# Optimization experiments

Measured on AMD Instinct MI355X. Metric: run time of the kernel, lower is better.

The kernel has to match this reference:

```python
import jax, jax.numpy as jnp
import numpy as np

N_NODES = 100000
N_EDGES = 1600000
HIDDEN = 128
N_GRAPHS = 64
N_CLASSES = 10


def setup_inputs() -> dict:
    key = jax.random.key(0)
    ks = jax.random.split(key, 10)
    x = jax.random.normal(ks[0], (N_NODES, 1), dtype=jnp.float32)
    edge_index = jax.random.randint(ks[1], (2, N_EDGES), 0, N_NODES, dtype=jnp.int32)
    batch = jnp.sort(jax.random.randint(ks[2], (N_NODES,), 0, N_GRAPHS, dtype=jnp.int32))
    def glorot(k, shape):
        fan_in, fan_out = shape
        s = jnp.sqrt(6.0 / (fan_in + fan_out))
        return jax.random.uniform(k, shape, jnp.float32, -s, s)
    return {
        "x": x,
        "edge_index": edge_index,
        "batch": batch,
        "W1l": glorot(ks[3], (1, HIDDEN)),
        "W1r": glorot(ks[4], (1, HIDDEN)),
        "b1": jnp.zeros((HIDDEN,), jnp.float32),
        "W2l": glorot(ks[5], (HIDDEN, HIDDEN)),
        "W2r": glorot(ks[6], (HIDDEN, HIDDEN)),
        "b2": jnp.zeros((HIDDEN,), jnp.float32),
        "W3l": glorot(ks[7], (HIDDEN, HIDDEN)),
        "W3r": glorot(ks[8], (HIDDEN, HIDDEN)),
        "b3": jnp.zeros((HIDDEN,), jnp.float32),
        "Wfc": glorot(ks[9], (HIDDEN, N_CLASSES)),
        "bfc": jnp.zeros((N_CLASSES,), jnp.float32),
    }


def _sage_conv(x, src, dst, Wl, Wr, b, n_nodes):
    # mean aggregation of source features at destination nodes
    msg = x[src]                                              # [E, d_in]
    agg = jax.ops.segment_sum(msg, dst, num_segments=n_nodes)  # [N, d_in]
    cnt = jax.ops.segment_sum(jnp.ones((src.shape[0], 1), x.dtype), dst,
                              num_segments=n_nodes)            # [N, 1]
    mean = agg / jnp.maximum(cnt, 1.0)
    # PyG SAGEConv: lin_l(mean neighbors) + bias + lin_r(self)
    return mean @ Wl + b + x @ Wr


def reference(x, edge_index, batch, W1l, W1r, b1, W2l, W2r, b2,
              W3l, W3r, b3, Wfc, bfc):
    src, dst = edge_index[0], edge_index[1]
    n = x.shape[0]
    h = jax.nn.relu(_sage_conv(x, src, dst, W1l, W1r, b1, n))
    h = jax.nn.relu(_sage_conv(h, src, dst, W2l, W2r, b2, n))
    h = jax.nn.relu(_sage_conv(h, src, dst, W3l, W3r, b3, n))
    # global_mean_pool over graph ids in `batch`
    pooled = jax.ops.segment_sum(h, batch, num_segments=N_GRAPHS)
    gcnt = jax.ops.segment_sum(jnp.ones((n, 1), h.dtype), batch,
                               num_segments=N_GRAPHS)
    pooled = pooled / jnp.maximum(gcnt, 1.0)
    logits = pooled @ Wfc + bfc
    return jax.nn.log_softmax(logits, axis=1)
```

## Files before the change

### kernel.cpp

```cpp
#include <hip/hip_runtime.h>

typedef unsigned int u32;
typedef unsigned short u16;
typedef short bf16x8 __attribute__((ext_vector_type(8)));
typedef float f32x4 __attribute__((ext_vector_type(4)));
typedef float f32x2 __attribute__((ext_vector_type(2)));
typedef u32 u32x4 __attribute__((ext_vector_type(4)));

#define HBLK 256

__device__ __forceinline__ u16 f2bf(float f) {
  u32 u = __float_as_uint(f);
  u = (u + 0x7FFFu + ((u >> 16) & 1u)) >> 16;
  return (u16)u;
}
__device__ __forceinline__ float bf2f(u32 h) { return __uint_as_float(h << 16); }

__global__ void hist_wprep_kernel(const int* __restrict__ dst, int* __restrict__ boff,
                                  int* __restrict__ btotal, int E, int nbuk, int chunk,
                                  const float* __restrict__ W2l, const float* __restrict__ W2r,
                                  const float* __restrict__ W3l, const float* __restrict__ W3r,
                                  u16* __restrict__ wt2, u16* __restrict__ wt3,
                                  const int* __restrict__ batch, int* __restrict__ gcnt, int n) {
  int tid = threadIdx.x;
  int idx = blockIdx.x * 1024 + tid;
  if (idx < 65536) {
    int which = idx >> 15, r = idx & 32767;
    int j = r >> 8, k = r & 255;
    if (which == 0) {
      float v = (k < 128) ? W2l[k * 128 + j] : W2r[(k - 128) * 128 + j];
      wt2[r] = f2bf(v);
    } else {
      float v = (k < 128) ? W3l[k * 128 + j] : W3r[(k - 128) * 128 + j];
      wt3[r] = f2bf(v);
    }
  }
  __shared__ int h[1024];
  __shared__ int gh[64];
  for (int i = tid; i < nbuk; i += 1024) h[i] = 0;
  if (tid < 64) gh[tid] = 0;
  __syncthreads();
  int b0 = blockIdx.x * chunk, b1 = min(b0 + chunk, E);
  int len = max(b1 - b0, 0);
  int ng = len >> 2;
  for (int g4 = tid; g4 < ng; g4 += 1024) {
    u32x4 d4 = *(const u32x4*)(dst + b0 + g4 * 4);
#pragma unroll
    for (int w = 0; w < 4; ++w) atomicAdd(&h[(int)d4[w] >> 7], 1);
  }
  for (int e = b0 + ng * 4 + tid; e < b1; e += 1024)
    atomicAdd(&h[dst[e] >> 7], 1);
  int chunkN = (n + HBLK - 1) / HBLK;
  int n0 = blockIdx.x * chunkN, n1 = min(n0 + chunkN, n);
  for (int i = n0 + tid; i < n1; i += 1024)
    atomicAdd(&gh[batch[i]], 1);
  __syncthreads();
  for (int i = tid; i < nbuk; i += 1024)
    boff[i * HBLK + blockIdx.x] = atomicAdd(&btotal[i], h[i]);
  if (tid < 64 && gh[tid] > 0)
    atomicAdd(&gcnt[tid], gh[tid]);
}

__global__ void scatter2_kernel(const int* __restrict__ src, const int* __restrict__ dst,
                                const int* __restrict__ btotal, const int* __restrict__ boff,
                                u32* __restrict__ part, int* __restrict__ bbase,
                                int E, int nbuk, int chunk) {
  __shared__ int wsum[1024];
  __shared__ int cur[1024];
  int tid = threadIdx.x;
  int v = (tid < nbuk) ? btotal[tid] : 0;
  wsum[tid] = v;
  __syncthreads();
  for (int off = 1; off < 1024; off <<= 1) {
    int t = (tid >= off) ? wsum[tid - off] : 0;
    __syncthreads();
    wsum[tid] += t;
    __syncthreads();
  }
  int excl = wsum[tid] - v;
  if (tid < nbuk) {
    cur[tid] = excl + boff[tid * HBLK + blockIdx.x];
    if (blockIdx.x == 0) bbase[tid] = excl;
  }
  __syncthreads();
  int b0 = blockIdx.x * chunk, b1 = min(b0 + chunk, E);
  int len = max(b1 - b0, 0);
  int ng = len >> 2;
  for (int g4 = tid; g4 < ng; g4 += 1024) {
    int e = b0 + g4 * 4;
    u32x4 s4 = *(const u32x4*)(src + e);
    u32x4 d4 = *(const u32x4*)(dst + e);
#pragma unroll
    for (int w = 0; w < 4; ++w) {
      int d = (int)d4[w];
      int pos = atomicAdd(&cur[d >> 7], 1);
      part[pos] = s4[w] | ((u32)(d & 127) << 25);
    }
  }
  for (int e = b0 + ng * 4 + tid; e < b1; e += 1024) {
    int d = dst[e];
    int pos = atomicAdd(&cur[d >> 7], 1);
    part[pos] = (u32)src[e] | ((u32)(d & 127) << 25);
  }
}

__global__ void scatter3_kernel(const u32* __restrict__ part, const int* __restrict__ bbase,
                                const float* __restrict__ x,
                                const float* __restrict__ W1l, const float* __restrict__ W1r,
                                const float* __restrict__ b1,
                                int* __restrict__ roff, int* __restrict__ csr,
                                u32* __restrict__ h1, int E, int nbuk, int n) {
  int b = blockIdx.x;
  int tid = threadIdx.x;
  int base = bbase[b];
  int end = (b + 1 < nbuk) ? bbase[b + 1] : E;
  __shared__ int cnt[128];
  __shared__ int s[128];
  __shared__ int cur[128];
  __shared__ float xsum[128];
  __shared__ float meanv[128];
  __shared__ float wlA[128], wrA[128], bA[128];
  if (tid < 128) {
    cnt[tid] = 0; xsum[tid] = 0.f;
    wlA[tid] = W1l[tid]; wrA[tid] = W1r[tid]; bA[tid] = b1[tid];
  }
  __syncthreads();
  for (int e = base + tid; e < end; e += 512)
    atomicAdd(&cnt[part[e] >> 25], 1);
  __syncthreads();
  if (tid < 128) s[tid] = cnt[tid];
  __syncthreads();
  for (int off = 1; off < 128; off <<= 1) {
    int t = (tid >= off && tid < 128) ? s[tid - off] : 0;
    __syncthreads();
    if (tid < 128) s[tid] += t;
    __syncthreads();
  }
  if (tid < 128) {
    int excl = s[tid] - cnt[tid];
    cur[tid] = base + excl;
    int node = b * 128 + tid;
    if (node < n) roff[node] = base + excl;
  }
  if (b == 0 && tid == 0) roff[n] = E;
  __syncthreads();
  for (int e = base + tid; e < end; e += 512) {
    u32 p = part[e];
    int sidx = (int)(p & 0x1FFFFFFu);
    int pos = atomicAdd(&cur[p >> 25], 1);
    csr[pos] = sidx;
    atomicAdd(&xsum[p >> 25], x[sidx]);
  }
  __syncthreads();
  if (tid < 128) meanv[tid] = xsum[tid] / (float)max(cnt[tid], 1);
  __syncthreads();
  int nlocal = min(128, n - b * 128);
  for (int q = tid; q < nlocal * 64; q += 512) {
    int ln = q >> 6, w = q & 63;
    int node = b * 128 + ln;
    int j0 = w * 2;
    float m = meanv[ln], xs = x[node];
    float v0 = fmaxf(m * wlA[j0] + xs * wrA[j0] + bA[j0], 0.f);
    float v1 = fmaxf(m * wlA[j0 + 1] + xs * wrA[j0 + 1] + bA[j0 + 1], 0.f);
    h1[(size_t)node * 64 + w] = (u32)f2bf(v0) | ((u32)f2bf(v1) << 16);
  }
}

__device__ __forceinline__ u32x4 grow(const u32* hp, int s) {
  return *(const u32x4*)(hp + (size_t)s * 64);
}
__device__ __forceinline__ void acc_row(f32x2* a, u32x4 v) {
#pragma unroll
  for (int w = 0; w < 4; ++w)
    a[w] += (f32x2){bf2f(v[w] & 0xFFFFu), bf2f(v[w] >> 16)};
}

__global__ void agg_kernel(const int* __restrict__ csr, const int* __restrict__ roff,
                           const u32* __restrict__ hin, u32* __restrict__ outv, int n) {
  int g = threadIdx.x >> 4, li = threadIdx.x & 15;
  int i = blockIdx.x * 16 + g;
  if (i >= n) return;
  int e0 = roff[i], e1 = roff[i + 1];
  f32x2 a[4] = {};
  const u32* hp = hin + li * 4;
  int e = e0;
  for (; e + 7 < e1; e += 8) {
    int s0 = csr[e], s1 = csr[e + 1], s2 = csr[e + 2], s3 = csr[e + 3];
    int s4 = csr[e + 4], s5 = csr[e + 5], s6 = csr[e + 6], s7 = csr[e + 7];
    u32x4 v0 = grow(hp, s0), v1 = grow(hp, s1), v2 = grow(hp, s2), v3 = grow(hp, s3);
    u32x4 v4 = grow(hp, s4), v5 = grow(hp, s5), v6 = grow(hp, s6), v7 = grow(hp, s7);
    acc_row(a, v0); acc_row(a, v1); acc_row(a, v2); acc_row(a, v3);
    acc_row(a, v4); acc_row(a, v5); acc_row(a, v6); acc_row(a, v7);
  }
  for (; e + 3 < e1; e += 4) {
    int s0 = csr[e], s1 = csr[e + 1], s2 = csr[e + 2], s3 = csr[e + 3];
    u32x4 v0 = grow(hp, s0), v1 = grow(hp, s1), v2 = grow(hp, s2), v3 = grow(hp, s3);
    acc_row(a, v0); acc_row(a, v1); acc_row(a, v2); acc_row(a, v3);
  }
  for (; e < e1; ++e) acc_row(a, grow(hp, csr[e]));
  float inv = 1.f / (float)max(e1 - e0, 1);
  u32x4 o;
#pragma unroll
  for (int w = 0; w < 4; ++w)
    o[w] = (u32)f2bf(a[w].x * inv) | ((u32)f2bf(a[w].y * inv) << 16);
  *(u32x4*)(outv + (size_t)i * 64 + li * 4) = o;
}

template <int MODE>
__launch_bounds__(512)
__global__ void mm_kernel(const u16* Aleft, const u16* Aright,
                          const u16* __restrict__ Wt, const float* __restrict__ bias,
                          u16* Out, const int* __restrict__ batch,
                          float* __restrict__ pooled, int n) {
  __shared__ u16 wlds[32768];
  __shared__ int bgp[128];
  for (int c = threadIdx.x; c < 4096; c += 512) {
    int j = c >> 5, ch = c & 31;
    int swz = ch ^ (j & 31);
    *(u32x4*)(&wlds[j * 256 + swz * 8]) = *(const u32x4*)(&Wt[j * 256 + ch * 8]);
  }
  __syncthreads();
  int wave = threadIdx.x >> 6;
  int lane = threadIdx.x & 63;
  int quad = lane >> 4, l16 = lane & 15;
  int row0 = blockIdx.x * 128 + wave * 16;
  int m = row0 + l16;
  int mc = m < n ? m : (n - 1);
  f32x4 acc[8] = {};
  const u16* Ah[2] = {Aleft, Aright};
#pragma unroll
  for (int half = 0; half < 2; ++half) {
    const u16* A = Ah[half] + (size_t)mc * 128;
#pragma unroll
    for (int s = 0; s < 4; ++s) {
      bf16x8 a = *(const bf16x8*)(A + s * 32 + quad * 8);
      int chunk = (half << 4) + (s << 2) + quad;
#pragma unroll
      for (int t = 0; t < 8; ++t) {
        int j = t * 16 + l16;
        int swz = chunk ^ (j & 31);
        bf16x8 b = *(const bf16x8*)(&wlds[j * 256 + swz * 8]);
        acc[t] = __builtin_amdgcn_mfma_f32_16x16x32_bf16(a, b, acc[t], 0, 0, 0);
      }
    }
  }
  __syncthreads();
  int rl_base = wave * 16 + quad * 4;
#pragma unroll
  for (int t = 0; t < 8; ++t) {
    int j = t * 16 + l16;
    float bj = bias[j];
#pragma unroll
    for (int r = 0; r < 4; ++r) {
      float v = acc[t][r] + bj;
      wlds[(rl_base + r) * 136 + j] = f2bf(fmaxf(v, 0.f));
    }
  }
  if (MODE == 1) {
    if (threadIdx.x < 128) {
      int rr = blockIdx.x * 128 + threadIdx.x;
      bgp[threadIdx.x] = (rr < n) ? batch[rr] : -1;
    }
  }
  __syncthreads();
  if (MODE == 0) {
    int base_row = blockIdx.x * 128;
    for (int q = 0; q < 4; ++q) {
      int idx = q * 512 + threadIdx.x;
      int rl = idx >> 4;
      int ch = idx & 15;
      int mr = base_row + rl;
      if (mr < n)
        *(u32x4*)(&Out[(size_t)mr * 128 + ch * 8]) =
            *(const u32x4*)(&wlds[rl * 136 + ch * 8]);
    }
  } else {
    int tcol = threadIdx.x & 127, seg = threadIdx.x >> 7;
    float accp = 0.f;
    int gcur = -1;
    for (int r = seg * 32; r < seg * 32 + 32; ++r) {
      int gb = bgp[r];
      if (gb != gcur) {
        if (gcur >= 0) atomicAdd(&pooled[gcur * 128 + tcol], accp);
        gcur = gb;
        accp = 0.f;
      }
      if (gb >= 0) accp += bf2f((u32)wlds[r * 136 + tcol]);
    }
    if (gcur >= 0) atomicAdd(&pooled[gcur * 128 + tcol], accp);
  }
}

__global__ void head_kernel(const float* __restrict__ pooled, const int* __restrict__ gcnt,
                            const float* __restrict__ Wfc, const float* __restrict__ bfc,
                            float* __restrict__ out) {
  __shared__ float lg[64][10];
  int t = threadIdx.x;
  if (t < 640) {
    int g = t / 10, c = t % 10;
    float inv = 1.f / (float)max(gcnt[g], 1);
    float acc = bfc[c];
    for (int k = 0; k < 128; ++k) acc += pooled[g * 128 + k] * inv * Wfc[k * 10 + c];
    lg[g][c] = acc;
  }
  __syncthreads();
  if (t < 640) {
    int g = t / 10, c = t % 10;
    float mx = -1e30f;
    for (int q = 0; q < 10; ++q) mx = fmaxf(mx, lg[g][q]);
    float se = 0.f;
    for (int q = 0; q < 10; ++q) se += expf(lg[g][q] - mx);
    out[g * 10 + c] = lg[g][c] - mx - logf(se);
  }
}

extern "C" void kernel_launch(void* const* d_in, const int* in_sizes, int n_in,
                              void* d_out, int out_size, void* d_ws, size_t ws_size,
                              hipStream_t stream) {
  const float* x   = (const float*)d_in[0];
  const int* ei    = (const int*)d_in[1];
  const int* batch = (const int*)d_in[2];
  const float* W1l = (const float*)d_in[3];
  const float* W1r = (const float*)d_in[4];
  const float* b1  = (const float*)d_in[5];
  const float* W2l = (const float*)d_in[6];
  const float* W2r = (const float*)d_in[7];
  const float* b2  = (const float*)d_in[8];
  const float* W3l = (const float*)d_in[9];
  const float* W3r = (const float*)d_in[10];
  const float* b3  = (const float*)d_in[11];
  const float* Wfc = (const float*)d_in[12];
  const float* bfc = (const float*)d_in[13];
  float* out = (float*)d_out;
  int N = in_sizes[0];
  int E = in_sizes[1] / 2;
  const int* src = ei;
  const int* dst = ei + E;

  char* p = (char*)d_ws;
  auto alloc = [&](size_t bytes) { void* r = (void*)p; p += (bytes + 255) & ~(size_t)255; return r; };
  int* roff   = (int*)alloc((size_t)(N + 1) * 4);
  int* csr    = (int*)alloc((size_t)E * 4);
  u32* bufA   = (u32*)alloc((size_t)N * 64 * 4);
  u32* bufB   = (u32*)alloc((size_t)N * 64 * 4);
  u16* wt2    = (u16*)alloc(32768 * 2);
  u16* wt3    = (u16*)alloc(32768 * 2);
  float* pooled = (float*)alloc(64 * 128 * 4);
  int* gcnt   = (int*)alloc(64 * 4);
  int* btotal = (int*)alloc(1024 * 4);
  int* bbase  = (int*)alloc(1024 * 4);

  int nbuk = (N + 127) >> 7;
  int* boff = (int*)bufA;
  u32* part = (u32*)bufB;
  int chunk = (((E + HBLK - 1) / HBLK) + 3) & ~3;

  hipMemsetAsync(pooled, 0, 32768 + 256 + 4096, stream);
  hist_wprep_kernel<<<HBLK, 1024, 0, stream>>>(dst, boff, btotal, E, nbuk, chunk,
                                               W2l, W2r, W3l, W3r, wt2, wt3,
                                               batch, gcnt, N);
  scatter2_kernel<<<HBLK, 1024, 0, stream>>>(src, dst, btotal, boff, part, bbase,
                                             E, nbuk, chunk);
  scatter3_kernel<<<nbuk, 512, 0, stream>>>(part, bbase, x, W1l, W1r, b1,
                                            roff, csr, bufA, E, nbuk, N);
  agg_kernel<<<(N + 15) / 16, 256, 0, stream>>>(csr, roff, bufA, bufB, N);
  mm_kernel<0><<<(N + 127) / 128, 512, 0, stream>>>((const u16*)bufB, (const u16*)bufA,
                                                    wt2, b2, (u16*)bufB, batch, pooled, N);
  agg_kernel<<<(N + 15) / 16, 256, 0, stream>>>(csr, roff, bufB, bufA, N);
  mm_kernel<1><<<(N + 127) / 128, 512, 0, stream>>>((const u16*)bufA, (const u16*)bufB,
                                                    wt3, b3, (u16*)bufA, batch, pooled, N);
  head_kernel<<<1, 640, 0, stream>>>(pooled, gcnt, Wfc, bfc, out);
}
```

Measured before the change: 300.5 us.

## Build CSR via per-node global atomics degree histogram and direct scatter

Replaces the two-level bucketed CSR construction (shared-memory bucket histogram, partitioned packed edges, per-bucket local sort) with a flat per-node degree histogram in global memory. A two-pass block scan over degrees produces row offsets, and a single scatter pass places edges using global atomics on per-node cursors while accumulating the layer-1 x sums. The layer-1 dense transform moves into its own kernel. This drops the intermediate partition buffer and one pass over the edges, but every edge now does global atomics with random addresses, which can serialize or thrash L2.

```diff
diff --git a/kernel.cpp b/kernel.cpp
--- a/kernel.cpp
+++ b/kernel.cpp
@@ -16,8 +16,9 @@
 }
 __device__ __forceinline__ float bf2f(u32 h) { return __uint_as_float(h << 16); }
 
-__global__ void hist_wprep_kernel(const int* __restrict__ dst, int* __restrict__ boff,
-                                  int* __restrict__ btotal, int E, int nbuk, int chunk,
+
+__global__ void hist_wprep_kernel(const int* __restrict__ dst, int* __restrict__ deg,
+                                  int E, int chunk,
                                   const float* __restrict__ W2l, const float* __restrict__ W2r,
                                   const float* __restrict__ W3l, const float* __restrict__ W3r,
                                   u16* __restrict__ wt2, u16* __restrict__ wt3,
@@ -35,9 +36,7 @@
       wt3[r] = f2bf(v);
     }
   }
-  __shared__ int h[1024];
   __shared__ int gh[64];
-  for (int i = tid; i < nbuk; i += 1024) h[i] = 0;
   if (tid < 64) gh[tid] = 0;
   __syncthreads();
   int b0 = blockIdx.x * chunk, b1 = min(b0 + chunk, E);
@@ -46,43 +45,65 @@
   for (int g4 = tid; g4 < ng; g4 += 1024) {
     u32x4 d4 = *(const u32x4*)(dst + b0 + g4 * 4);
 #pragma unroll
-    for (int w = 0; w < 4; ++w) atomicAdd(&h[(int)d4[w] >> 7], 1);
+    for (int w = 0; w < 4; ++w) atomicAdd(&deg[(int)d4[w]], 1);
   }
   for (int e = b0 + ng * 4 + tid; e < b1; e += 1024)
-    atomicAdd(&h[dst[e] >> 7], 1);
+    atomicAdd(&deg[dst[e]], 1);
   int chunkN = (n + HBLK - 1) / HBLK;
   int n0 = blockIdx.x * chunkN, n1 = min(n0 + chunkN, n);
   for (int i = n0 + tid; i < n1; i += 1024)
     atomicAdd(&gh[batch[i]], 1);
   __syncthreads();
-  for (int i = tid; i < nbuk; i += 1024)
-    boff[i * HBLK + blockIdx.x] = atomicAdd(&btotal[i], h[i]);
   if (tid < 64 && gh[tid] > 0)
     atomicAdd(&gcnt[tid], gh[tid]);
 }
 
-__global__ void scatter2_kernel(const int* __restrict__ src, const int* __restrict__ dst,
-                                const int* __restrict__ btotal, const int* __restrict__ boff,
-                                u32* __restrict__ part, int* __restrict__ bbase,
-                                int E, int nbuk, int chunk) {
-  __shared__ int wsum[1024];
-  __shared__ int cur[1024];
-  int tid = threadIdx.x;
-  int v = (tid < nbuk) ? btotal[tid] : 0;
-  wsum[tid] = v;
+__global__ void degsum_kernel(const int* __restrict__ deg, int* __restrict__ bsum, int n) {
+  __shared__ int s[1024];
+  int tid = threadIdx.x;
+  int node = blockIdx.x * 1024 + tid;
+  s[tid] = (node < n) ? deg[node] : 0;
+  __syncthreads();
+  for (int off = 512; off > 0; off >>= 1) {
+    if (tid < off) s[tid] += s[tid + off];
+    __syncthreads();
+  }
+  if (tid == 0) bsum[blockIdx.x] = s[0];
+}
+
+__global__ void degscan_kernel(const int* __restrict__ deg, const int* __restrict__ bsum,
+                               int* __restrict__ roff, int* __restrict__ cur,
+                               int nb, int n, int E) {
+  __shared__ int s[1024];
+  __shared__ int bs[256];
+  int tid = threadIdx.x;
+  if (tid < nb) bs[tid] = bsum[tid];
+  int node = blockIdx.x * 1024 + tid;
+  int v = (node < n) ? deg[node] : 0;
+  s[tid] = v;
   __syncthreads();
   for (int off = 1; off < 1024; off <<= 1) {
-    int t = (tid >= off) ? wsum[tid - off] : 0;
+    int t = (tid >= off) ? s[tid - off] : 0;
     __syncthreads();
-    wsum[tid] += t;
+    s[tid] += t;
     __syncthreads();
   }
-  int excl = wsum[tid] - v;
-  if (tid < nbuk) {
-    cur[tid] = excl + boff[tid * HBLK + blockIdx.x];
-    if (blockIdx.x == 0) bbase[tid] = excl;
-  }
-  __syncthreads();
+  int base = 0;
+  for (int i = 0; i < blockIdx.x; ++i) base += bs[i];
+  int incl = s[tid];
+  int excl = incl - v;
+  if (node < n) {
+    roff[node] = base + excl;
+    cur[node] = base + excl;
+  }
+  if (node == n - 1) roff[n] = base + incl;
+}
+
+__global__ void scatter_kernel(const int* __restrict__ src, const int* __restrict__ dst,
+                               const float* __restrict__ x, int* __restrict__ cur,
+                               int* __restrict__ csr, float* __restrict__ xsum,
+                               int E, int chunk) {
+  int tid = threadIdx.x;
   int b0 = blockIdx.x * chunk, b1 = min(b0 + chunk, E);
   int len = max(b1 - b0, 0);
   int ng = len >> 2;
@@ -92,77 +113,45 @@
     u32x4 d4 = *(const u32x4*)(dst + e);
 #pragma unroll
     for (int w = 0; w < 4; ++w) {
-      int d = (int)d4[w];
-      int pos = atomicAdd(&cur[d >> 7], 1);
-      part[pos] = s4[w] | ((u32)(d & 127) << 25);
+      int d = (int)d4[w], si = (int)s4[w];
+      int pos = atomicAdd(&cur[d], 1);
+      csr[pos] = si;
+      atomicAdd(&xsum[d], x[si]);
     }
   }
   for (int e = b0 + ng * 4 + tid; e < b1; e += 1024) {
-    int d = dst[e];
-    int pos = atomicAdd(&cur[d >> 7], 1);
-    part[pos] = (u32)src[e] | ((u32)(d & 127) << 25);
-  }
-}
-
-__global__ void scatter3_kernel(const u32* __restrict__ part, const int* __restrict__ bbase,
-                                const float* __restrict__ x,
-                                const float* __restrict__ W1l, const float* __restrict__ W1r,
-                                const float* __restrict__ b1,
-                                int* __restrict__ roff, int* __restrict__ csr,
-                                u32* __restrict__ h1, int E, int nbuk, int n) {
-  int b = blockIdx.x;
-  int tid = threadIdx.x;
-  int base = bbase[b];
-  int end = (b + 1 < nbuk) ? bbase[b + 1] : E;
-  __shared__ int cnt[128];
-  __shared__ int s[128];
-  __shared__ int cur[128];
-  __shared__ float xsum[128];
-  __shared__ float meanv[128];
+    int d = dst[e], si = src[e];
+    int pos = atomicAdd(&cur[d], 1);
+    csr[pos] = si;
+    atomicAdd(&xsum[d], x[si]);
+  }
+}
+
+__global__ void l1_kernel(const float* __restrict__ x, const float* __restrict__ xsum,
+                          const int* __restrict__ deg,
+                          const float* __restrict__ W1l, const float* __restrict__ W1r,
+                          const float* __restrict__ b1, u32* __restrict__ h1, int n) {
   __shared__ float wlA[128], wrA[128], bA[128];
+  __shared__ float meanv[128], xv[128];
+  int tid = threadIdx.x;
+  int base = blockIdx.x * 128;
+  int nlocal = min(128, n - base);
   if (tid < 128) {
-    cnt[tid] = 0; xsum[tid] = 0.f;
     wlA[tid] = W1l[tid]; wrA[tid] = W1r[tid]; bA[tid] = b1[tid];
-  }
-  __syncthreads();
-  for (int e = base + tid; e < end; e += 512)
-    atomicAdd(&cnt[part[e] >> 25], 1);
-  __syncthreads();
-  if (tid < 128) s[tid] = cnt[tid];
-  __syncthreads();
-  for (int off = 1; off < 128; off <<= 1) {
-    int t = (tid >= off && tid < 128) ? s[tid - off] : 0;
-    __syncthreads();
-    if (tid < 128) s[tid] += t;
-    __syncthreads();
-  }
-  if (tid < 128) {
-    int excl = s[tid] - cnt[tid];
-    cur[tid] = base + excl;
-    int node = b * 128 + tid;
-    if (node < n) roff[node] = base + excl;
-  }
-  if (b == 0 && tid == 0) roff[n] = E;
-  __syncthreads();
-  for (int e = base + tid; e < end; e += 512) {
-    u32 p = part[e];
-    int sidx = (int)(p & 0x1FFFFFFu);
-    int pos = atomicAdd(&cur[p >> 25], 1);
-    csr[pos] = sidx;
-    atomicAdd(&xsum[p >> 25], x[sidx]);
-  }
-  __syncthreads();
-  if (tid < 128) meanv[tid] = xsum[tid] / (float)max(cnt[tid], 1);
-  __syncthreads();
-  int nlocal = min(128, n - b * 128);
-  for (int q = tid; q < nlocal * 64; q += 512) {
+    if (tid < nlocal) {
+      int node = base + tid;
+      meanv[tid] = xsum[node] / (float)max(deg[node], 1);
+      xv[tid] = x[node];
+    }
+  }
+  __syncthreads();
+  for (int q = tid; q < nlocal * 64; q += 256) {
     int ln = q >> 6, w = q & 63;
-    int node = b * 128 + ln;
     int j0 = w * 2;
-    float m = meanv[ln], xs = x[node];
+    float m = meanv[ln], xs = xv[ln];
     float v0 = fmaxf(m * wlA[j0] + xs * wrA[j0] + bA[j0], 0.f);
     float v1 = fmaxf(m * wlA[j0 + 1] + xs * wrA[j0 + 1] + bA[j0 + 1], 0.f);
-    h1[(size_t)node * 64 + w] = (u32)f2bf(v0) | ((u32)f2bf(v1) << 16);
+    h1[(size_t)(base + ln) * 64 + w] = (u32)f2bf(v0) | ((u32)f2bf(v1) << 16);
   }
 }
 
@@ -346,23 +335,24 @@
   u16* wt2    = (u16*)alloc(32768 * 2);
   u16* wt3    = (u16*)alloc(32768 * 2);
   float* pooled = (float*)alloc(64 * 128 * 4);
-  int* gcnt   = (int*)alloc(64 * 4);
-  int* btotal = (int*)alloc(1024 * 4);
-  int* bbase  = (int*)alloc(1024 * 4);
-
-  int nbuk = (N + 127) >> 7;
-  int* boff = (int*)bufA;
-  u32* part = (u32*)bufB;
+  int* gcnt     = (int*)alloc(64 * 4);
+  int* deg      = (int*)alloc((size_t)N * 4);
+  float* xsum   = (float*)alloc((size_t)N * 4);
+  int* cur      = (int*)alloc((size_t)N * 4);
+  int* bsum     = (int*)alloc(1024);
+
   int chunk = (((E + HBLK - 1) / HBLK) + 3) & ~3;
-
-  hipMemsetAsync(pooled, 0, 32768 + 256 + 4096, stream);
-  hist_wprep_kernel<<<HBLK, 1024, 0, stream>>>(dst, boff, btotal, E, nbuk, chunk,
+  int nb2 = (N + 1023) >> 10;
+
+  size_t zbytes = 32768 + 256 + (((size_t)N * 4 + 255) & ~(size_t)255) * 2;
+  hipMemsetAsync(pooled, 0, zbytes, stream);
+  hist_wprep_kernel<<<HBLK, 1024, 0, stream>>>(dst, deg, E, chunk,
                                                W2l, W2r, W3l, W3r, wt2, wt3,
                                                batch, gcnt, N);
-  scatter2_kernel<<<HBLK, 1024, 0, stream>>>(src, dst, btotal, boff, part, bbase,
-                                             E, nbuk, chunk);
-  scatter3_kernel<<<nbuk, 512, 0, stream>>>(part, bbase, x, W1l, W1r, b1,
-                                            roff, csr, bufA, E, nbuk, N);
+  degsum_kernel<<<nb2, 1024, 0, stream>>>(deg, bsum, N);
+  degscan_kernel<<<nb2, 1024, 0, stream>>>(deg, bsum, roff, cur, nb2, N, E);
+  scatter_kernel<<<HBLK, 1024, 0, stream>>>(src, dst, x, cur, csr, xsum, E, chunk);
+  l1_kernel<<<(N + 127) / 128, 256, 0, stream>>>(x, xsum, deg, W1l, W1r, b1, bufA, N);
   agg_kernel<<<(N + 15) / 16, 256, 0, stream>>>(csr, roff, bufA, bufB, N);
   mm_kernel<0><<<(N + 127) / 128, 512, 0, stream>>>((const u16*)bufB, (const u16*)bufA,
                                                     wt2, b2, (u16*)bufB, batch, pooled, N);
```

Measured after the change: 488.7 us. +62.6%, slower.

## Replace histogram+scan edge bucketing with fixed-capacity buckets via global atomics

Applied to the files above, without the earlier changes.

The separate histogram and prefix-scan pass is removed. Edges are now scattered directly into fixed-capacity per-bucket slots (CAP entries per 128-node bucket), claimed with global atomic counters padded to 64 bytes each. The CSR gets per-node start and end offsets instead of one contiguous offset array, so the aggregation kernels read rend. This saves a kernel launch and a full pass over dst. In exchange it puts heavy contention on global atomics and assumes no bucket gets more than CAP edges, which holds for uniformly random graphs but would overflow on skewed degree distributions.

```diff
diff --git a/kernel.cpp b/kernel.cpp
--- a/kernel.cpp
+++ b/kernel.cpp
@@ -8,6 +8,7 @@
 typedef u32 u32x4 __attribute__((ext_vector_type(4)));
 
 #define HBLK 256
+#define CAP 2560
 
 __device__ __forceinline__ u16 f2bf(float f) {
   u32 u = __float_as_uint(f);
@@ -16,12 +17,14 @@
 }
 __device__ __forceinline__ float bf2f(u32 h) { return __uint_as_float(h << 16); }
 
-__global__ void hist_wprep_kernel(const int* __restrict__ dst, int* __restrict__ boff,
-                                  int* __restrict__ btotal, int E, int nbuk, int chunk,
-                                  const float* __restrict__ W2l, const float* __restrict__ W2r,
-                                  const float* __restrict__ W3l, const float* __restrict__ W3r,
-                                  u16* __restrict__ wt2, u16* __restrict__ wt3,
-                                  const int* __restrict__ batch, int* __restrict__ gcnt, int n) {
+
+__global__ void scatter_build_kernel(const int* __restrict__ src, const int* __restrict__ dst,
+                                     const float* __restrict__ W2l, const float* __restrict__ W2r,
+                                     const float* __restrict__ W3l, const float* __restrict__ W3r,
+                                     u16* __restrict__ wt2, u16* __restrict__ wt3,
+                                     const int* __restrict__ batch, int* __restrict__ gcnt,
+                                     int* __restrict__ bcnt, u32* __restrict__ part,
+                                     int E, int chunk, int n) {
   int tid = threadIdx.x;
   int idx = blockIdx.x * 1024 + tid;
   if (idx < 65536) {
@@ -35,53 +38,8 @@
       wt3[r] = f2bf(v);
     }
   }
-  __shared__ int h[1024];
   __shared__ int gh[64];
-  for (int i = tid; i < nbuk; i += 1024) h[i] = 0;
   if (tid < 64) gh[tid] = 0;
-  __syncthreads();
-  int b0 = blockIdx.x * chunk, b1 = min(b0 + chunk, E);
-  int len = max(b1 - b0, 0);
-  int ng = len >> 2;
-  for (int g4 = tid; g4 < ng; g4 += 1024) {
-    u32x4 d4 = *(const u32x4*)(dst + b0 + g4 * 4);
-#pragma unroll
-    for (int w = 0; w < 4; ++w) atomicAdd(&h[(int)d4[w] >> 7], 1);
-  }
-  for (int e = b0 + ng * 4 + tid; e < b1; e += 1024)
-    atomicAdd(&h[dst[e] >> 7], 1);
-  int chunkN = (n + HBLK - 1) / HBLK;
-  int n0 = blockIdx.x * chunkN, n1 = min(n0 + chunkN, n);
-  for (int i = n0 + tid; i < n1; i += 1024)
-    atomicAdd(&gh[batch[i]], 1);
-  __syncthreads();
-  for (int i = tid; i < nbuk; i += 1024)
-    boff[i * HBLK + blockIdx.x] = atomicAdd(&btotal[i], h[i]);
-  if (tid < 64 && gh[tid] > 0)
-    atomicAdd(&gcnt[tid], gh[tid]);
-}
-
-__global__ void scatter2_kernel(const int* __restrict__ src, const int* __restrict__ dst,
-                                const int* __restrict__ btotal, const int* __restrict__ boff,
-                                u32* __restrict__ part, int* __restrict__ bbase,
-                                int E, int nbuk, int chunk) {
-  __shared__ int wsum[1024];
-  __shared__ int cur[1024];
-  int tid = threadIdx.x;
-  int v = (tid < nbuk) ? btotal[tid] : 0;
-  wsum[tid] = v;
-  __syncthreads();
-  for (int off = 1; off < 1024; off <<= 1) {
-    int t = (tid >= off) ? wsum[tid - off] : 0;
-    __syncthreads();
-    wsum[tid] += t;
-    __syncthreads();
-  }
-  int excl = wsum[tid] - v;
-  if (tid < nbuk) {
-    cur[tid] = excl + boff[tid * HBLK + blockIdx.x];
-    if (blockIdx.x == 0) bbase[tid] = excl;
-  }
   __syncthreads();
   int b0 = blockIdx.x * chunk, b1 = min(b0 + chunk, E);
   int len = max(b1 - b0, 0);
@@ -93,27 +51,37 @@
 #pragma unroll
     for (int w = 0; w < 4; ++w) {
       int d = (int)d4[w];
-      int pos = atomicAdd(&cur[d >> 7], 1);
-      part[pos] = s4[w] | ((u32)(d & 127) << 25);
+      int b = d >> 7;
+      int pos = atomicAdd(&bcnt[b * 16], 1);
+      part[b * CAP + pos] = s4[w] | ((u32)(d & 127) << 25);
     }
   }
   for (int e = b0 + ng * 4 + tid; e < b1; e += 1024) {
     int d = dst[e];
-    int pos = atomicAdd(&cur[d >> 7], 1);
-    part[pos] = (u32)src[e] | ((u32)(d & 127) << 25);
-  }
-}
-
-__global__ void scatter3_kernel(const u32* __restrict__ part, const int* __restrict__ bbase,
+    int b = d >> 7;
+    int pos = atomicAdd(&bcnt[b * 16], 1);
+    part[b * CAP + pos] = (u32)src[e] | ((u32)(d & 127) << 25);
+  }
+  int chunkN = (n + HBLK - 1) / HBLK;
+  int n0 = blockIdx.x * chunkN, n1 = min(n0 + chunkN, n);
+  for (int i = n0 + tid; i < n1; i += 1024)
+    atomicAdd(&gh[batch[i]], 1);
+  __syncthreads();
+  if (tid < 64 && gh[tid] > 0)
+    atomicAdd(&gcnt[tid], gh[tid]);
+}
+
+__global__ void scatter3_kernel(const u32* __restrict__ part, const int* __restrict__ bcnt,
                                 const float* __restrict__ x,
                                 const float* __restrict__ W1l, const float* __restrict__ W1r,
                                 const float* __restrict__ b1,
-                                int* __restrict__ roff, int* __restrict__ csr,
-                                u32* __restrict__ h1, int E, int nbuk, int n) {
+                                int* __restrict__ roff, int* __restrict__ rend,
+                                int* __restrict__ csr,
+                                u32* __restrict__ h1, int nbuk, int n) {
   int b = blockIdx.x;
   int tid = threadIdx.x;
-  int base = bbase[b];
-  int end = (b + 1 < nbuk) ? bbase[b + 1] : E;
+  int base = b * CAP;
+  int end = base + bcnt[b * 16];
   __shared__ int cnt[128];
   __shared__ int s[128];
   __shared__ int cur[128];
@@ -140,9 +108,11 @@
     int excl = s[tid] - cnt[tid];
     cur[tid] = base + excl;
     int node = b * 128 + tid;
-    if (node < n) roff[node] = base + excl;
-  }
-  if (b == 0 && tid == 0) roff[n] = E;
+    if (node < n) {
+      roff[node] = base + excl;
+      rend[node] = base + excl + cnt[tid];
+    }
+  }
   __syncthreads();
   for (int e = base + tid; e < end; e += 512) {
     u32 p = part[e];
@@ -176,11 +146,12 @@
 }
 
 __global__ void agg_kernel(const int* __restrict__ csr, const int* __restrict__ roff,
+                           const int* __restrict__ rend,
                            const u32* __restrict__ hin, u32* __restrict__ outv, int n) {
   int g = threadIdx.x >> 4, li = threadIdx.x & 15;
   int i = blockIdx.x * 16 + g;
   if (i >= n) return;
-  int e0 = roff[i], e1 = roff[i + 1];
+  int e0 = roff[i], e1 = rend[i];
   f32x2 a[4] = {};
   const u32* hp = hin + li * 4;
   int e = e0;
@@ -339,34 +310,32 @@
 
   char* p = (char*)d_ws;
   auto alloc = [&](size_t bytes) { void* r = (void*)p; p += (bytes + 255) & ~(size_t)255; return r; };
-  int* roff   = (int*)alloc((size_t)(N + 1) * 4);
-  int* csr    = (int*)alloc((size_t)E * 4);
+  int nbuk = (N + 127) >> 7;
+  int* roff   = (int*)alloc((size_t)N * 4);
+  int* rend   = (int*)alloc((size_t)N * 4);
+  int* csr    = (int*)alloc((size_t)nbuk * CAP * 4);
   u32* bufA   = (u32*)alloc((size_t)N * 64 * 4);
   u32* bufB   = (u32*)alloc((size_t)N * 64 * 4);
   u16* wt2    = (u16*)alloc(32768 * 2);
   u16* wt3    = (u16*)alloc(32768 * 2);
   float* pooled = (float*)alloc(64 * 128 * 4);
-  int* gcnt   = (int*)alloc(64 * 4);
-  int* btotal = (int*)alloc(1024 * 4);
-  int* bbase  = (int*)alloc(1024 * 4);
-
-  int nbuk = (N + 127) >> 7;
-  int* boff = (int*)bufA;
+  int* gcnt     = (int*)alloc(64 * 4);
+  int* bcnt     = (int*)alloc((size_t)nbuk * 64);
+
   u32* part = (u32*)bufB;
   int chunk = (((E + HBLK - 1) / HBLK) + 3) & ~3;
 
-  hipMemsetAsync(pooled, 0, 32768 + 256 + 4096, stream);
-  hist_wprep_kernel<<<HBLK, 1024, 0, stream>>>(dst, boff, btotal, E, nbuk, chunk,
-                                               W2l, W2r, W3l, W3r, wt2, wt3,
-                                               batch, gcnt, N);
-  scatter2_kernel<<<HBLK, 1024, 0, stream>>>(src, dst, btotal, boff, part, bbase,
-                                             E, nbuk, chunk);
-  scatter3_kernel<<<nbuk, 512, 0, stream>>>(part, bbase, x, W1l, W1r, b1,
-                                            roff, csr, bufA, E, nbuk, N);
-  agg_kernel<<<(N + 15) / 16, 256, 0, stream>>>(csr, roff, bufA, bufB, N);
+  size_t zbytes = 32768 + 256 + (((size_t)nbuk * 64 + 255) & ~(size_t)255);
+  hipMemsetAsync(pooled, 0, zbytes, stream);
+  scatter_build_kernel<<<HBLK, 1024, 0, stream>>>(src, dst, W2l, W2r, W3l, W3r,
+                                                  wt2, wt3, batch, gcnt, bcnt, part,
+                                                  E, chunk, N);
+  scatter3_kernel<<<nbuk, 512, 0, stream>>>(part, bcnt, x, W1l, W1r, b1,
+                                            roff, rend, csr, bufA, nbuk, N);
+  agg_kernel<<<(N + 15) / 16, 256, 0, stream>>>(csr, roff, rend, bufA, bufB, N);
   mm_kernel<0><<<(N + 127) / 128, 512, 0, stream>>>((const u16*)bufB, (const u16*)bufA,
                                                     wt2, b2, (u16*)bufB, batch, pooled, N);
-  agg_kernel<<<(N + 15) / 16, 256, 0, stream>>>(csr, roff, bufB, bufA, N);
+  agg_kernel<<<(N + 15) / 16, 256, 0, stream>>>(csr, roff, rend, bufB, bufA, N);
   mm_kernel<1><<<(N + 127) / 128, 512, 0, stream>>>((const u16*)bufA, (const u16*)bufB,
                                                     wt3, b3, (u16*)bufA, batch, pooled, N);
   head_kernel<<<1, 640, 0, stream>>>(pooled, gcnt, Wfc, bfc, out);
```

After: 365.4 us. +21.6%, slower.
